# Kernel optimization log

Measured on AMD Instinct MI355X. Metric: run time of the kernel, lower is better.

Reference implementation:

```python
import jax, jax.numpy as jnp
import numpy as np


def setup_inputs() -> dict:
    key = jax.random.key(0)
    k1, k2 = jax.random.split(key)
    B, L, D = 16, 2048, 1024
    sentout = jax.random.normal(k1, (B, L, D), dtype=jnp.float32)
    nl_input = jax.random.randint(k2, (B, L), 0, 4, dtype=jnp.int64)
    return {"sentout": sentout, "nl_input": nl_input}


def reference(sentout, nl_input):
    # Per batch row: stable partition of sentout rows -- positions where
    # nl_input != 0 first (in original order), then positions where == 0.
    # Equivalent to tf.gather_nd(where(!=0)) ++ tf.gather_nd(where(==0)).
    # A stable argsort on the key (is_padding: 0 for facts, 1 for pads)
    # produces exactly this permutation, fully vectorized over the batch.
    is_pad = (nl_input == 0).astype(jnp.int32)          # [B, L]
    order = jnp.argsort(is_pad, axis=1, stable=True)    # [B, L]
    # Gather encoded facts in the partitioned order: [B, L, D]
    return jnp.take_along_axis(sentout, order[:, :, None], axis=1)
```

## Files before the change

### kernel.cpp

```cpp
#include <hip/hip_runtime.h>

constexpr int L_CONST = 2048;
constexpr int D_CONST = 1024;
constexpr int NT      = 256;
constexpr int PER     = L_CONST / NT;
constexpr int ROWS    = 16;
constexpr int GROUPS  = L_CONST / ROWS;
constexpr int D4      = D_CONST / 4;

typedef float floatx4 __attribute__((ext_vector_type(4)));

__global__ __launch_bounds__(NT) void fused_partition_gather(
    const float* __restrict__ in, const int* __restrict__ nl,
    float* __restrict__ out) {
    const int b = blockIdx.x / GROUPS;
    const int g = blockIdx.x % GROUPS;
    const int t = threadIdx.x;

    const int4* row4 = (const int4*)(nl + (size_t)b * L_CONST);
    int4 v0 = row4[t * 2];
    int4 v1 = row4[t * 2 + 1];
    int flags[PER];
    flags[0] = (v0.x != 0); flags[1] = (v0.y != 0);
    flags[2] = (v0.z != 0); flags[3] = (v0.w != 0);
    flags[4] = (v1.x != 0); flags[5] = (v1.y != 0);
    flags[6] = (v1.z != 0); flags[7] = (v1.w != 0);
    int cnt = 0;
    #pragma unroll
    for (int k = 0; k < PER; ++k) cnt += flags[k];

    __shared__ int s[NT];
    __shared__ int lds_order[L_CONST];
    s[t] = cnt;
    __syncthreads();
    #pragma unroll
    for (int off = 1; off < NT; off <<= 1) {
        int add = (t >= off) ? s[t - off] : 0;
        __syncthreads();
        s[t] += add;
        __syncthreads();
    }
    const int incl     = s[t];
    const int totalNon = s[NT - 1];
    const int exclNon  = incl - cnt;

    int run = 0;
    #pragma unroll
    for (int k = 0; k < PER; ++k) {
        const int j        = t * PER + k;
        const int npPrefix = exclNon + run;
        const int dest = flags[k] ? npPrefix : (totalNon + (j - npPrefix));
        lds_order[dest] = j;
        run += flags[k];
    }
    __syncthreads();

    int srcs[ROWS];
    #pragma unroll
    for (int r = 0; r < ROWS; ++r) srcs[r] = lds_order[g * ROWS + r];

    const floatx4* inb  = (const floatx4*)in + (size_t)b * L_CONST * D4;
    floatx4*       outb = (floatx4*)out      + ((size_t)b * L_CONST + (size_t)g * ROWS) * D4;
    #pragma unroll
    for (int r = 0; r < ROWS; ++r) {
        floatx4 v = inb[(size_t)srcs[r] * D4 + t];
        __builtin_nontemporal_store(v, &outb[r * D4 + t]);
    }
}

extern "C" void kernel_launch(void* const* d_in, const int* in_sizes, int n_in,
                              void* d_out, int out_size, void* d_ws, size_t ws_size,
                              hipStream_t stream) {
    const float* sentout = (const float*)d_in[0];
    const int*   nl      = (const int*)d_in[1];
    float*       out     = (float*)d_out;

    const int B = in_sizes[1] / L_CONST;
    fused_partition_gather<<<B * GROUPS, NT, 0, stream>>>(sentout, nl, out);
}
```

Measured before the change: 45.40 us.

## Switch to source-indexed scatter and issue input loads before the prefix scan

Each block now reads its 16 contiguous source rows up front, before the flag scan, so the global load latency overlaps with the LDS scan work. It then computes only the destination indices of its own rows and scatters them to the output, instead of building the full 2048-entry order table and gathering. Holding 16 float4 values per thread raises register pressure, and the occupancy hint of 4 blocks may limit registers further. The writes become scattered by row, but each row is still written contiguously.

```diff
diff --git a/kernel.cpp b/kernel.cpp
--- a/kernel.cpp
+++ b/kernel.cpp
@@ -10,7 +10,7 @@
 
 typedef float floatx4 __attribute__((ext_vector_type(4)));
 
-__global__ __launch_bounds__(NT) void fused_partition_gather(
+__global__ __launch_bounds__(NT, 4) void fused_src_partition(
     const float* __restrict__ in, const int* __restrict__ nl,
     float* __restrict__ out) {
     const int b = blockIdx.x / GROUPS;
@@ -18,19 +18,28 @@
     const int t = threadIdx.x;
 
     const int4* row4 = (const int4*)(nl + (size_t)b * L_CONST);
-    int4 v0 = row4[t * 2];
-    int4 v1 = row4[t * 2 + 1];
+    int4 f0 = row4[t * 2];
+    int4 f1 = row4[t * 2 + 1];
+
+    const floatx4* inb = (const floatx4*)in
+                       + ((size_t)b * L_CONST + (size_t)g * ROWS) * D4;
+    floatx4 v[ROWS];
+    #pragma unroll
+    for (int r = 0; r < ROWS; ++r) v[r] = inb[r * D4 + t];
+
+    __builtin_amdgcn_sched_barrier(0);
+
     int flags[PER];
-    flags[0] = (v0.x != 0); flags[1] = (v0.y != 0);
-    flags[2] = (v0.z != 0); flags[3] = (v0.w != 0);
-    flags[4] = (v1.x != 0); flags[5] = (v1.y != 0);
-    flags[6] = (v1.z != 0); flags[7] = (v1.w != 0);
+    flags[0] = (f0.x != 0); flags[1] = (f0.y != 0);
+    flags[2] = (f0.z != 0); flags[3] = (f0.w != 0);
+    flags[4] = (f1.x != 0); flags[5] = (f1.y != 0);
+    flags[6] = (f1.z != 0); flags[7] = (f1.w != 0);
     int cnt = 0;
     #pragma unroll
     for (int k = 0; k < PER; ++k) cnt += flags[k];
 
     __shared__ int s[NT];
-    __shared__ int lds_order[L_CONST];
+    __shared__ int dstL[ROWS];
     s[t] = cnt;
     __syncthreads();
     #pragma unroll
@@ -44,27 +53,23 @@
     const int totalNon = s[NT - 1];
     const int exclNon  = incl - cnt;
 
+    const int j0 = g * ROWS;
     int run = 0;
     #pragma unroll
     for (int k = 0; k < PER; ++k) {
         const int j        = t * PER + k;
         const int npPrefix = exclNon + run;
-        const int dest = flags[k] ? npPrefix : (totalNon + (j - npPrefix));
-        lds_order[dest] = j;
+        if (j >= j0 && j < j0 + ROWS) {
+            dstL[j - j0] = flags[k] ? npPrefix : (totalNon + (j - npPrefix));
+        }
         run += flags[k];
     }
     __syncthreads();
 
-    int srcs[ROWS];
-    #pragma unroll
-    for (int r = 0; r < ROWS; ++r) srcs[r] = lds_order[g * ROWS + r];
-
-    const floatx4* inb  = (const floatx4*)in + (size_t)b * L_CONST * D4;
-    floatx4*       outb = (floatx4*)out      + ((size_t)b * L_CONST + (size_t)g * ROWS) * D4;
+    floatx4* outB = (floatx4*)out + (size_t)b * L_CONST * D4;
     #pragma unroll
     for (int r = 0; r < ROWS; ++r) {
-        floatx4 v = inb[(size_t)srcs[r] * D4 + t];
-        __builtin_nontemporal_store(v, &outb[r * D4 + t]);
+        __builtin_nontemporal_store(v[r], outB + (size_t)dstL[r] * D4 + t);
     }
 }
 
@@ -76,5 +81,5 @@
     float*       out     = (float*)d_out;
 
     const int B = in_sizes[1] / L_CONST;
-    fused_partition_gather<<<B * GROUPS, NT, 0, stream>>>(sentout, nl, out);
+    fused_src_partition<<<B * GROUPS, NT, 0, stream>>>(sentout, nl, out);
 }
```

Result: faster. 43.77 us (-3.6%).
